# Kernel optimization log

Hardware: AMD Instinct MI355X
Metric: run time of the kernel (lower is better)

## Reference

```python
import jax, jax.numpy as jnp
import numpy as np

B = 2048
NUM_FEATURES = 40960
M = 256
N = 32
K = 32
MAX_EVAL = 10000.0  # Chess_Lib.MAX_EVAL stand-in
SPARSITY = 32.0 / NUM_FEATURES  # ~32 active HalfKP features per position


def _xavier(key, shape):
    fan_out, fan_in = shape
    limit = np.sqrt(6.0 / (fan_in + fan_out)).astype(np.float32)
    return jax.random.uniform(key, shape, jnp.float32, -limit, limit)


def setup_inputs() -> dict:
    key = jax.random.key(0)
    ks = jax.random.split(key, 8)
    # ~32-hot sparse binary feature vectors (HalfKP style)
    wf = (jax.random.uniform(ks[0], (B, NUM_FEATURES)) < SPARSITY).astype(jnp.float32)
    bf = (jax.random.uniform(ks[1], (B, NUM_FEATURES)) < SPARSITY).astype(jnp.float32)
    stm = jnp.round(jax.random.uniform(ks[2], (B, 1))).astype(jnp.float32)
    return {
        "white_features": wf,
        "black_features": bf,
        "stm": stm,
        "ft_w": _xavier(ks[3], (M, NUM_FEATURES)),
        "ft_b": jnp.zeros((M,), jnp.float32),
        "l1_w": _xavier(ks[4], (N, 2 * M)),
        "l1_b": jnp.zeros((N,), jnp.float32),
        "l2_w": _xavier(ks[5], (K, N)),
        "l2_b": jnp.zeros((K,), jnp.float32),
        "l3_w": _xavier(ks[6], (1, K)),
        "l3_b": jnp.zeros((1,), jnp.float32),
    }


def reference(white_features, black_features, stm, ft_w, ft_b,
              l1_w, l1_b, l2_w, l2_b, l3_w, l3_b):
    # feature transformer: [B,F] @ [F,M] -> [B,M]
    w = white_features @ ft_w.T + ft_b
    b = black_features @ ft_w.T + ft_b
    acc = stm * jnp.concatenate([w, b], axis=1) + (1.0 - stm) * jnp.concatenate([b, w], axis=1)
    l1_x = jnp.clip(acc, 0.0, 1.0)
    l2_x = jnp.clip(l1_x @ l1_w.T + l1_b, 0.0, 1.0)
    l3_x = jnp.clip(l2_x @ l2_w.T + l2_b, 0.0, 1.0)
    ev = jnp.clip(l3_x @ l3_w.T + l3_b, 0.0, 1.0)
    # align_eval without the python int() cast (kept batched/differentiable)
    return (ev - 0.5) * 2.0 * MAX_EVAL
```

## Files before the change

### kernel.cpp

```cpp
#include <hip/hip_runtime.h>
#include <hip/hip_bf16.h>

#define NF 40960
#define MD 256
#define BATCH 2048
#define CAP 512
#define CAPB 128
#define NTILE ((NF / 64) * (MD / 64))
#define NROWS (2 * BATCH)

typedef float vf4 __attribute__((ext_vector_type(4)));
typedef unsigned int vu4 __attribute__((ext_vector_type(4)));

__device__ __forceinline__ float clip01(float v) {
    return fminf(fmaxf(v, 0.0f), 1.0f);
}

__global__ __launch_bounds__(256, 4) void nnue_scan(
    const float* __restrict__ wf, const float* __restrict__ bfeat,
    int* __restrict__ cnt, int* __restrict__ idxg)
{
    __shared__ int lidx[CAPB];
    __shared__ int lcnt;
    const int g = blockIdx.x;
    const int t = threadIdx.x;
    const int pos = g & (BATCH - 1);
    const int color = g >> 11;

    if (t == 0) lcnt = 0;
    __syncthreads();

    const vu4* src = (const vu4*)((color ? bfeat : wf) + (size_t)pos * NF);

    unsigned int mask[5];
    #pragma unroll
    for (int w = 0; w < 5; ++w) {
        unsigned int acc = 0;
        #pragma unroll
        for (int q = 0; q < 8; ++q) {
            vu4 v = src[t + (w * 8 + q) * 256];
            unsigned int nib = ((v.x >> 29) & 1u)
                             | (((v.y >> 29) & 1u) << 1)
                             | (((v.z >> 29) & 1u) << 2)
                             | (((v.w >> 29) & 1u) << 3);
            acc |= nib << (4 * q);
        }
        mask[w] = acc;
    }

    if (mask[0] | mask[1] | mask[2] | mask[3] | mask[4]) {
        #pragma unroll
        for (int w = 0; w < 5; ++w) {
            unsigned int x = mask[w];
            while (x) {
                const int b = __builtin_ctz(x);
                x &= x - 1;
                const int k = w * 8 + (b >> 2);
                const int fi = 4 * (t + k * 256) + (b & 3);
                const int p = atomicAdd(&lcnt, 1);
                if (p < CAPB) lidx[p] = fi;
            }
        }
    }
    __syncthreads();

    const int n = min(lcnt, CAPB);
    for (int j = t; j < n; j += 256) idxg[(size_t)g * CAPB + j] = lidx[j];
    if (t == 0) cnt[g] = n;
}

__global__ __launch_bounds__(256, 2) void transpose_ft2(
    const float* __restrict__ in, float* __restrict__ outT)
{
    __shared__ float tile[256][65];
    const int b = blockIdx.x;
    const int t = threadIdx.x;
    const int f0 = b * 64;
    if (b == 0) outT[(size_t)NF * MD + t] = 0.0f;

    const int tx = t & 63;
    const int ty = t >> 6;
    #pragma unroll 8
    for (int r = ty; r < 256; r += 4)
        tile[r][tx] = in[(size_t)r * NF + f0 + tx];
    __syncthreads();
    #pragma unroll 8
    for (int r = 0; r < 64; ++r)
        outT[(size_t)(f0 + r) * MD + t] = tile[t][r];
}

struct GSmem {
    int iw[CAPB + 8], ib[CAPB + 8];
    float xsh[512];
    float red[32][9];
    float ysh[32], zsh[32];
};

__global__ __launch_bounds__(256, 4) void nnue_gather(
    const float* __restrict__ ftT,
    const int* __restrict__ cnt, const int* __restrict__ idxg,
    const float* __restrict__ ft_b, const float* __restrict__ stm,
    const float* __restrict__ l1_w, const float* __restrict__ l1_b,
    const float* __restrict__ l2_w, const float* __restrict__ l2_b,
    const float* __restrict__ l3_w, const float* __restrict__ l3_b,
    float* __restrict__ out)
{
    __shared__ GSmem s;
    const int pos = blockIdx.x;
    const int t = threadIdx.x;

    const int cw = min(cnt[pos], CAPB);
    const int cb = min(cnt[BATCH + pos], CAPB);
    const int m = (max(cw, cb) + 7) & ~7;

    for (int j = t; j < cw; j += 256) s.iw[j] = idxg[(size_t)pos * CAPB + j];
    for (int j = t; j < cb; j += 256) s.ib[j] = idxg[(size_t)(BATCH + pos) * CAPB + j];
    for (int j = cw + t; j < m; j += 256) s.iw[j] = NF;
    for (int j = cb + t; j < m; j += 256) s.ib[j] = NF;
    __syncthreads();

    const float bias = ft_b[t];
    float aw = 0.0f, ab = 0.0f;
    for (int j = 0; j < m; j += 8) {
        float vw[8], vb[8];
        #pragma unroll
        for (int q = 0; q < 8; ++q) vw[q] = ftT[(size_t)s.iw[j + q] * MD + t];
        #pragma unroll
        for (int q = 0; q < 8; ++q) vb[q] = ftT[(size_t)s.ib[j + q] * MD + t];
        aw += ((vw[0] + vw[1]) + (vw[2] + vw[3])) + ((vw[4] + vw[5]) + (vw[6] + vw[7]));
        ab += ((vb[0] + vb[1]) + (vb[2] + vb[3])) + ((vb[4] + vb[5]) + (vb[6] + vb[7]));
    }
    const float accW = bias + aw;
    const float accB = bias + ab;

    const float sv = stm[pos];
    s.xsh[t]       = clip01(sv * accW + (1.0f - sv) * accB);
    s.xsh[256 + t] = clip01(sv * accB + (1.0f - sv) * accW);
    __syncthreads();
    {
        const int n = t & 31;
        const int c = t >> 5;
        const float* w1 = l1_w + (size_t)n * 512 + c * 64;
        const float* xx = s.xsh + c * 64;
        float p = 0.0f;
        #pragma unroll
        for (int j = 0; j < 64; ++j) p += xx[j] * w1[j];
        s.red[n][c] = p;
    }
    __syncthreads();
    if (t < 32) {
        float v = l1_b[t];
        #pragma unroll
        for (int c = 0; c < 8; ++c) v += s.red[t][c];
        s.ysh[t] = clip01(v);
    }
    __syncthreads();
    if (t < 32) {
        float v = l2_b[t];
        const float* w2 = l2_w + t * 32;
        #pragma unroll
        for (int j = 0; j < 32; ++j) v += s.ysh[j] * w2[j];
        s.zsh[t] = clip01(v);
    }
    __syncthreads();
    if (t == 0) {
        float v = l3_b[0];
        #pragma unroll
        for (int j = 0; j < 32; ++j) v += s.zsh[j] * l3_w[j];
        out[pos] = (clip01(v) - 0.5f) * 20000.0f;
    }
}

__global__ __launch_bounds__(256) void transpose_ft(const float* __restrict__ in,
                                                    float* __restrict__ outT) {
    __shared__ float tile[64][65];
    const int b = blockIdx.x;
    const int t = threadIdx.x;
    const int f0 = (b % (NF / 64)) * 64;
    const int m0 = (b / (NF / 64)) * 64;
    const int tx = t & 63;
    const int ty = t >> 6;
    #pragma unroll
    for (int r = ty; r < 64; r += 4)
        tile[r][tx] = in[(size_t)(m0 + r) * NF + f0 + tx];
    __syncthreads();
    #pragma unroll
    for (int r = ty; r < 64; r += 4)
        outT[(size_t)(f0 + r) * MD + m0 + tx] = tile[tx][r];
}

struct ScanSmem {
    int idxW[CAP], idxB[CAP];
    int nW, nB;
    float xsh[512];
    float red[32][9];
    float ysh[32], zsh[32];
};
union Smem {
    float tile[64][65];
    ScanSmem s;
};

__device__ __forceinline__ void scan_pos(ScanSmem& s, int t, int pos,
    const float* __restrict__ wf, const float* __restrict__ bfeat)
{
    if (t == 0) { s.nW = 0; s.nB = 0; }
    __syncthreads();
    const vf4* wf4 = (const vf4*)(wf + (size_t)pos * NF);
    const vf4* bf4 = (const vf4*)(bfeat + (size_t)pos * NF);
    #pragma unroll 4
    for (int i = t; i < NF / 4; i += 256) {
        vf4 v = wf4[i];
        if (v.x + v.y + v.z + v.w != 0.0f) {
            if (v.x != 0.0f) { int p = atomicAdd(&s.nW, 1); if (p < CAP) s.idxW[p] = 4 * i;     }
            if (v.y != 0.0f) { int p = atomicAdd(&s.nW, 1); if (p < CAP) s.idxW[p] = 4 * i + 1; }
            if (v.z != 0.0f) { int p = atomicAdd(&s.nW, 1); if (p < CAP) s.idxW[p] = 4 * i + 2; }
            if (v.w != 0.0f) { int p = atomicAdd(&s.nW, 1); if (p < CAP) s.idxW[p] = 4 * i + 3; }
        }
        vf4 uu = bf4[i];
        if (uu.x + uu.y + uu.z + uu.w != 0.0f) {
            if (uu.x != 0.0f) { int p = atomicAdd(&s.nB, 1); if (p < CAP) s.idxB[p] = 4 * i;     }
            if (uu.y != 0.0f) { int p = atomicAdd(&s.nB, 1); if (p < CAP) s.idxB[p] = 4 * i + 1; }
            if (uu.z != 0.0f) { int p = atomicAdd(&s.nB, 1); if (p < CAP) s.idxB[p] = 4 * i + 2; }
            if (uu.w != 0.0f) { int p = atomicAdd(&s.nB, 1); if (p < CAP) s.idxB[p] = 4 * i + 3; }
        }
    }
    __syncthreads();
}

__device__ __forceinline__ void gather_tail(ScanSmem& s, int t, int pos,
    const float* __restrict__ gt, int transposed,
    const float* __restrict__ ft_b, const float* __restrict__ stm,
    const float* __restrict__ l1_w, const float* __restrict__ l1_b,
    const float* __restrict__ l2_w, const float* __restrict__ l2_b,
    const float* __restrict__ l3_w, const float* __restrict__ l3_b,
    float* __restrict__ out)
{
    const int cw = min(s.nW, CAP);
    const int cb = min(s.nB, CAP);

    float accW = ft_b[t];
    float accB = ft_b[t];
    if (transposed) {
        for (int j = 0; j < cw; ++j) accW += gt[(size_t)s.idxW[j] * MD + t];
        for (int j = 0; j < cb; ++j) accB += gt[(size_t)s.idxB[j] * MD + t];
    } else {
        const float* row = gt + (size_t)t * NF;
        for (int j = 0; j < cw; ++j) accW += row[s.idxW[j]];
        for (int j = 0; j < cb; ++j) accB += row[s.idxB[j]];
    }

    const float sv = stm[pos];
    s.xsh[t]       = clip01(sv * accW + (1.0f - sv) * accB);
    s.xsh[256 + t] = clip01(sv * accB + (1.0f - sv) * accW);
    __syncthreads();

    {
        const int n = t & 31;
        const int c = t >> 5;
        const float* w1 = l1_w + (size_t)n * 512 + c * 64;
        const float* xx = s.xsh + c * 64;
        float p = 0.0f;
        #pragma unroll
        for (int j = 0; j < 64; ++j) p += xx[j] * w1[j];
        s.red[n][c] = p;
    }
    __syncthreads();
    if (t < 32) {
        float v = l1_b[t];
        #pragma unroll
        for (int c = 0; c < 8; ++c) v += s.red[t][c];
        s.ysh[t] = clip01(v);
    }
    __syncthreads();
    if (t < 32) {
        float v = l2_b[t];
        const float* w2 = l2_w + t * 32;
        #pragma unroll
        for (int j = 0; j < 32; ++j) v += s.ysh[j] * w2[j];
        s.zsh[t] = clip01(v);
    }
    __syncthreads();
    if (t == 0) {
        float v = l3_b[0];
        #pragma unroll
        for (int j = 0; j < 32; ++j) v += s.zsh[j] * l3_w[j];
        out[pos] = (clip01(v) - 0.5f) * 20000.0f;
    }
}

__global__ __launch_bounds__(256) void nnue_plain(
    const float* __restrict__ wf, const float* __restrict__ bfeat,
    const float* __restrict__ stm, const float* __restrict__ gt,
    const float* __restrict__ ft_b,
    const float* __restrict__ l1_w, const float* __restrict__ l1_b,
    const float* __restrict__ l2_w, const float* __restrict__ l2_b,
    const float* __restrict__ l3_w, const float* __restrict__ l3_b,
    float* __restrict__ out, int transposed)
{
    __shared__ Smem u;
    const int pos = blockIdx.x;
    const int t = threadIdx.x;
    scan_pos(u.s, t, pos, wf, bfeat);
    gather_tail(u.s, t, pos, gt, transposed, ft_b, stm,
                l1_w, l1_b, l2_w, l2_b, l3_w, l3_b, out);
}

extern "C" void kernel_launch(void* const* d_in, const int* in_sizes, int n_in,
                              void* d_out, int out_size, void* d_ws, size_t ws_size,
                              hipStream_t stream) {
    const float* wf    = (const float*)d_in[0];
    const float* bfeat = (const float*)d_in[1];
    const float* stm   = (const float*)d_in[2];
    const float* ft_w  = (const float*)d_in[3];
    const float* ft_b  = (const float*)d_in[4];
    const float* l1_w  = (const float*)d_in[5];
    const float* l1_b  = (const float*)d_in[6];
    const float* l2_w  = (const float*)d_in[7];
    const float* l2_b  = (const float*)d_in[8];
    const float* l3_w  = (const float*)d_in[9];
    const float* l3_b  = (const float*)d_in[10];
    float* out = (float*)d_out;

    float* ftT = (float*)d_ws;
    int* cnt  = (int*)((float*)d_ws + (size_t)(NF + 1) * MD);
    int* idxg = cnt + NROWS;
    const size_t needFull = (size_t)(NF + 1) * MD * sizeof(float)
                          + (size_t)NROWS * sizeof(int)
                          + (size_t)NROWS * CAPB * sizeof(int);
    const size_t needT = (size_t)NF * MD * sizeof(float);

    if (ws_size >= needFull) {
        nnue_scan<<<NROWS, 256, 0, stream>>>(wf, bfeat, cnt, idxg);
        transpose_ft2<<<NF / 64, 256, 0, stream>>>(ft_w, ftT);
        nnue_gather<<<BATCH, 256, 0, stream>>>(
            ftT, cnt, idxg, ft_b, stm,
            l1_w, l1_b, l2_w, l2_b, l3_w, l3_b, out);
        return;
    }

    if (ws_size >= needT) {
        transpose_ft<<<NTILE, 256, 0, stream>>>(ft_w, ftT);
        nnue_plain<<<BATCH, 256, 0, stream>>>(
            wf, bfeat, stm, ftT, ft_b,
            l1_w, l1_b, l2_w, l2_b, l3_w, l3_b, out, 1);
    } else {
        nnue_plain<<<BATCH, 256, 0, stream>>>(
            wf, bfeat, stm, ft_w, ft_b,
            l1_w, l1_b, l2_w, l2_b, l3_w, l3_b, out, 0);
    }
}
```

Baseline: 698.7 us.

## Fuse sparse feature scan into gather kernel, drop index workspace round-trip

Merges the separate scan kernel, which built per-row active-feature index lists in global memory, into the gather/MLP kernel. Each block now scans both white and black feature rows directly into shared memory, then gathers and runs the MLP. Loads of the dense feature rows switch to nontemporal loads. This removes a kernel launch and the global write/read of count and index arrays. The cost is that each block now streams two full rows, so the scan runs with half as many blocks and less parallelism.

```diff
diff --git a/kernel.cpp b/kernel.cpp
--- a/kernel.cpp
+++ b/kernel.cpp
@@ -16,105 +16,108 @@
     return fminf(fmaxf(v, 0.0f), 1.0f);
 }
 
-__global__ __launch_bounds__(256, 4) void nnue_scan(
+__global__ __launch_bounds__(256, 2) void transpose_ft2(
+    const float* __restrict__ in, float* __restrict__ outT)
+{
+    __shared__ float tile[256][65];
+    const int b = blockIdx.x;
+    const int t = threadIdx.x;
+    const int f0 = b * 64;
+    if (b == 0) outT[(size_t)NF * MD + t] = 0.0f;
+
+    const int tx = t & 63;
+    const int ty = t >> 6;
+    #pragma unroll 8
+    for (int r = ty; r < 256; r += 4)
+        tile[r][tx] = in[(size_t)r * NF + f0 + tx];
+    __syncthreads();
+    #pragma unroll 8
+    for (int r = 0; r < 64; ++r)
+        outT[(size_t)(f0 + r) * MD + t] = tile[t][r];
+}
+
+struct FSmem {
+    int iw[CAPB + 8], ib[CAPB + 8];
+    int nw, nb;
+    float xsh[512];
+    float red[32][9];
+    float ysh[32], zsh[32];
+};
+
+__global__ __launch_bounds__(256, 4) void nnue_fused(
     const float* __restrict__ wf, const float* __restrict__ bfeat,
-    int* __restrict__ cnt, int* __restrict__ idxg)
-{
-    __shared__ int lidx[CAPB];
-    __shared__ int lcnt;
-    const int g = blockIdx.x;
+    const float* __restrict__ ftT,
+    const float* __restrict__ ft_b, const float* __restrict__ stm,
+    const float* __restrict__ l1_w, const float* __restrict__ l1_b,
+    const float* __restrict__ l2_w, const float* __restrict__ l2_b,
+    const float* __restrict__ l3_w, const float* __restrict__ l3_b,
+    float* __restrict__ out)
+{
+    __shared__ FSmem s;
+    const int pos = blockIdx.x;
     const int t = threadIdx.x;
-    const int pos = g & (BATCH - 1);
-    const int color = g >> 11;
-
-    if (t == 0) lcnt = 0;
-    __syncthreads();
-
-    const vu4* src = (const vu4*)((color ? bfeat : wf) + (size_t)pos * NF);
-
-    unsigned int mask[5];
+    if (t == 0) { s.nw = 0; s.nb = 0; }
+    __syncthreads();
+
+    const vu4* srcW = (const vu4*)(wf + (size_t)pos * NF);
+    const vu4* srcB = (const vu4*)(bfeat + (size_t)pos * NF);
+
+    unsigned int mw[5], mb[5];
     #pragma unroll
     for (int w = 0; w < 5; ++w) {
-        unsigned int acc = 0;
+        unsigned int aW = 0, aB = 0;
         #pragma unroll
         for (int q = 0; q < 8; ++q) {
-            vu4 v = src[t + (w * 8 + q) * 256];
-            unsigned int nib = ((v.x >> 29) & 1u)
-                             | (((v.y >> 29) & 1u) << 1)
-                             | (((v.z >> 29) & 1u) << 2)
-                             | (((v.w >> 29) & 1u) << 3);
-            acc |= nib << (4 * q);
-        }
-        mask[w] = acc;
-    }
-
-    if (mask[0] | mask[1] | mask[2] | mask[3] | mask[4]) {
+            vu4 v = __builtin_nontemporal_load(srcW + t + (w * 8 + q) * 256);
+            aW |= (((v.x >> 29) & 1u)
+                 | (((v.y >> 29) & 1u) << 1)
+                 | (((v.z >> 29) & 1u) << 2)
+                 | (((v.w >> 29) & 1u) << 3)) << (4 * q);
+        }
+        #pragma unroll
+        for (int q = 0; q < 8; ++q) {
+            vu4 v = __builtin_nontemporal_load(srcB + t + (w * 8 + q) * 256);
+            aB |= (((v.x >> 29) & 1u)
+                 | (((v.y >> 29) & 1u) << 1)
+                 | (((v.z >> 29) & 1u) << 2)
+                 | (((v.w >> 29) & 1u) << 3)) << (4 * q);
+        }
+        mw[w] = aW; mb[w] = aB;
+    }
+
+    if (mw[0] | mw[1] | mw[2] | mw[3] | mw[4]) {
         #pragma unroll
         for (int w = 0; w < 5; ++w) {
-            unsigned int x = mask[w];
+            unsigned int x = mw[w];
             while (x) {
                 const int b = __builtin_ctz(x);
                 x &= x - 1;
                 const int k = w * 8 + (b >> 2);
                 const int fi = 4 * (t + k * 256) + (b & 3);
-                const int p = atomicAdd(&lcnt, 1);
-                if (p < CAPB) lidx[p] = fi;
+                const int p = atomicAdd(&s.nw, 1);
+                if (p < CAPB) s.iw[p] = fi;
             }
         }
     }
-    __syncthreads();
-
-    const int n = min(lcnt, CAPB);
-    for (int j = t; j < n; j += 256) idxg[(size_t)g * CAPB + j] = lidx[j];
-    if (t == 0) cnt[g] = n;
-}
-
-__global__ __launch_bounds__(256, 2) void transpose_ft2(
-    const float* __restrict__ in, float* __restrict__ outT)
-{
-    __shared__ float tile[256][65];
-    const int b = blockIdx.x;
-    const int t = threadIdx.x;
-    const int f0 = b * 64;
-    if (b == 0) outT[(size_t)NF * MD + t] = 0.0f;
-
-    const int tx = t & 63;
-    const int ty = t >> 6;
-    #pragma unroll 8
-    for (int r = ty; r < 256; r += 4)
-        tile[r][tx] = in[(size_t)r * NF + f0 + tx];
-    __syncthreads();
-    #pragma unroll 8
-    for (int r = 0; r < 64; ++r)
-        outT[(size_t)(f0 + r) * MD + t] = tile[t][r];
-}
-
-struct GSmem {
-    int iw[CAPB + 8], ib[CAPB + 8];
-    float xsh[512];
-    float red[32][9];
-    float ysh[32], zsh[32];
-};
-
-__global__ __launch_bounds__(256, 4) void nnue_gather(
-    const float* __restrict__ ftT,
-    const int* __restrict__ cnt, const int* __restrict__ idxg,
-    const float* __restrict__ ft_b, const float* __restrict__ stm,
-    const float* __restrict__ l1_w, const float* __restrict__ l1_b,
-    const float* __restrict__ l2_w, const float* __restrict__ l2_b,
-    const float* __restrict__ l3_w, const float* __restrict__ l3_b,
-    float* __restrict__ out)
-{
-    __shared__ GSmem s;
-    const int pos = blockIdx.x;
-    const int t = threadIdx.x;
-
-    const int cw = min(cnt[pos], CAPB);
-    const int cb = min(cnt[BATCH + pos], CAPB);
+    if (mb[0] | mb[1] | mb[2] | mb[3] | mb[4]) {
+        #pragma unroll
+        for (int w = 0; w < 5; ++w) {
+            unsigned int x = mb[w];
+            while (x) {
+                const int b = __builtin_ctz(x);
+                x &= x - 1;
+                const int k = w * 8 + (b >> 2);
+                const int fi = 4 * (t + k * 256) + (b & 3);
+                const int p = atomicAdd(&s.nb, 1);
+                if (p < CAPB) s.ib[p] = fi;
+            }
+        }
+    }
+    __syncthreads();
+
+    const int cw = min(s.nw, CAPB);
+    const int cb = min(s.nb, CAPB);
     const int m = (max(cw, cb) + 7) & ~7;
-
-    for (int j = t; j < cw; j += 256) s.iw[j] = idxg[(size_t)pos * CAPB + j];
-    for (int j = t; j < cb; j += 256) s.ib[j] = idxg[(size_t)(BATCH + pos) * CAPB + j];
     for (int j = cw + t; j < m; j += 256) s.iw[j] = NF;
     for (int j = cb + t; j < m; j += 256) s.ib[j] = NF;
     __syncthreads();
@@ -323,18 +326,13 @@
     float* out = (float*)d_out;
 
     float* ftT = (float*)d_ws;
-    int* cnt  = (int*)((float*)d_ws + (size_t)(NF + 1) * MD);
-    int* idxg = cnt + NROWS;
-    const size_t needFull = (size_t)(NF + 1) * MD * sizeof(float)
-                          + (size_t)NROWS * sizeof(int)
-                          + (size_t)NROWS * CAPB * sizeof(int);
-    const size_t needT = (size_t)NF * MD * sizeof(float);
+    const size_t needFull = (size_t)(NF + 1) * MD * sizeof(float);
+    const size_t needT    = (size_t)NF * MD * sizeof(float);
 
     if (ws_size >= needFull) {
-        nnue_scan<<<NROWS, 256, 0, stream>>>(wf, bfeat, cnt, idxg);
         transpose_ft2<<<NF / 64, 256, 0, stream>>>(ft_w, ftT);
-        nnue_gather<<<BATCH, 256, 0, stream>>>(
-            ftT, cnt, idxg, ft_b, stm,
+        nnue_fused<<<BATCH, 256, 0, stream>>>(
+            wf, bfeat, ftT, ft_b, stm,
             l1_w, l1_b, l2_w, l2_b, l3_w, l3_b, out);
         return;
     }
```

New measurement: 698.7 us. Within noise of the previous version (+0.0%).
